# Kernel tuning notes

Hardware: AMD Instinct MI355X
Metric: run time of the kernel (lower is better)

The kernel has to match this reference:

```python
import jax, jax.numpy as jnp
import numpy as np

L, C, H, FF = 12, 768, 12, 3072
DH = C // H
VOCAB = 30522
B, P, T = 64, 196, 40
PATCH_FLAT = 768  # 16*16*3
MAXP, MAXW = P + 1, T + 2


def _ln(x, w, b, eps):
    m = jnp.mean(x, axis=-1, keepdims=True)
    v = jnp.mean(jnp.square(x - m), axis=-1, keepdims=True)
    return (x - m) * jax.lax.rsqrt(v + eps) * w + b


def setup_inputs() -> dict:
    key = jax.random.key(0)
    ks = iter(jax.random.split(key, 40))
    s = 0.02
    rn = lambda shape: jax.random.normal(next(ks), shape, jnp.float32) * s
    return {
        'vis_in': jax.random.normal(next(ks), (B, P, PATCH_FLAT), jnp.float32),
        'txt_in': jax.random.randint(next(ks), (B, T), 0, VOCAB),
        'vis_mask': jnp.ones((B, P), jnp.int32),
        'txt_mask': jnp.ones((B, T), jnp.int32),
        'patch_w': rn((C, PATCH_FLAT)), 'patch_b': jnp.zeros((C,), jnp.float32),
        'w_embed': rn((VOCAB, C)),
        't_pos': rn((MAXW, C)),
        'v_pos': rn((1, MAXP, C)),
        'v_cls': rn((1, 1, C)),
        'v_mod': rn((1, 1, C)), 't_mod': rn((1, 1, C)),
        'vn_w': jnp.ones((C,), jnp.float32), 'vn_b': jnp.zeros((C,), jnp.float32),
        'tn_w': jnp.ones((C,), jnp.float32), 'tn_b': jnp.zeros((C,), jnp.float32),
        'qkv_w': rn((L, 3 * C, C)), 'qkv_b': jnp.zeros((L, 3 * C), jnp.float32),
        'proj_w': rn((L, C, C)), 'proj_b': jnp.zeros((L, C), jnp.float32),
        'n1_w': jnp.ones((L, C), jnp.float32), 'n1_b': jnp.zeros((L, C), jnp.float32),
        'n2_w': jnp.ones((L, C), jnp.float32), 'n2_b': jnp.zeros((L, C), jnp.float32),
        'fc1_w': rn((L, FF, C)), 'fc1_b': jnp.zeros((L, FF), jnp.float32),
        'fc2_w': rn((L, C, FF)), 'fc2_b': jnp.zeros((L, C), jnp.float32),
    }


def reference(vis_in, txt_in, vis_mask, txt_mask, patch_w, patch_b, w_embed, t_pos,
              v_pos, v_cls, v_mod, t_mod, vn_w, vn_b, tn_w, tn_b, qkv_w, qkv_b,
              proj_w, proj_b, n1_w, n1_b, n2_w, n2_b, fc1_w, fc1_b, fc2_w, fc2_b):
    Bsz = vis_in.shape[0]
    # patch projection and word embedding
    v_emb = vis_in @ patch_w.T + patch_b                      # [B, P, C]
    t_emb = w_embed[txt_in]                                    # [B, T, C]
    v_emb = jnp.concatenate([jnp.broadcast_to(v_cls, (Bsz, 1, C)), v_emb], axis=1)
    VL = v_emb.shape[1]                                        # P + 1
    v_emb = _ln(v_emb + v_pos[:, :VL] + v_mod, vn_w, vn_b, 1e-5)
    t_emb = _ln(t_emb + t_pos[:T] + t_mod, tn_w, tn_b, 1e-5)
    x = jnp.concatenate([t_emb, v_emb], axis=1)                # [B, N, C], N = T+1+P
    m = jnp.concatenate([txt_mask, jnp.ones((Bsz, 1), txt_mask.dtype), vis_mask], axis=-1)
    # pairwise mask: attn_mask[b,i,j] == 0 -> masked (broadcast over heads)
    masked = (m[:, None, :, None] * m[:, None, None, :]) == 0  # [B,1,N,N]
    scale = DH ** -0.5
    for l in range(L):
        h = _ln(x, n1_w[l], n1_b[l], 1e-6)
        qkv = (h @ qkv_w[l].T + qkv_b[l]).reshape(Bsz, -1, 3, H, DH)
        q = jnp.transpose(qkv[:, :, 0], (0, 2, 1, 3))          # [B,H,N,DH]
        k = jnp.transpose(qkv[:, :, 1], (0, 2, 1, 3))
        v = jnp.transpose(qkv[:, :, 2], (0, 2, 1, 3))
        attn = jnp.einsum('bhqd,bhkd->bhqk', q, k) * scale
        attn = jnp.where(masked, jnp.asarray(-1e30, attn.dtype), attn)
        attn = jax.nn.softmax(attn, axis=-1)
        o = jnp.einsum('bhqk,bhkd->bhqd', attn, v)
        o = jnp.transpose(o, (0, 2, 1, 3)).reshape(Bsz, -1, C)
        x = x + (o @ proj_w[l].T + proj_b[l])
        h2 = _ln(x, n2_w[l], n2_b[l], 1e-6)
        h2 = jax.nn.gelu(h2 @ fc1_w[l].T + fc1_b[l], approximate=False)
        x = x + (h2 @ fc2_w[l].T + fc2_b[l])
    return x
```

## Files before the change

### kernel.cpp

```cpp
#include <hip/hip_runtime.h>
#include <hip/hip_bf16.h>

using bf16 = __hip_bfloat16;
typedef __bf16 bfv8 __attribute__((ext_vector_type(8)));
typedef float f32x4 __attribute__((ext_vector_type(4)));

#define DEVI __device__ __forceinline__

constexpr int L_ = 12, C_ = 768, H_ = 12, FF_ = 3072, DH_ = 64;
constexpr int B_ = 64, P_ = 196, T_ = 40;
constexpr int N_ = T_ + 1 + P_;
constexpr int M_ = B_ * N_;
constexpr int MPAD = 15360;
constexpr int NKV = 256;
constexpr int BP_ = B_ * P_;

constexpr size_t OFF_X   = 0;
constexpr size_t SZ_X    = (size_t)MPAD * C_ * 4;
constexpr size_t OFF_H   = OFF_X + SZ_X;
constexpr size_t SZ_H    = (size_t)MPAD * C_ * 2;
constexpr size_t OFF_Q   = OFF_H + SZ_H;
constexpr size_t SZ_QKV1 = (size_t)B_ * H_ * NKV * DH_ * 2;
constexpr size_t OFF_K   = OFF_Q + SZ_QKV1;
constexpr size_t OFF_V   = OFF_K + SZ_QKV1;
constexpr size_t OFF_O   = OFF_V + SZ_QKV1;
constexpr size_t SZ_O    = SZ_H;
constexpr size_t OFF_FFH = OFF_O + SZ_O;
constexpr size_t SZ_FFH  = (size_t)MPAD * FF_ * 2;
constexpr size_t OFF_WB  = OFF_FFH + SZ_FFH;
constexpr size_t SZ_WB   = (size_t)(2304 + 768 + 3072 + 3072) * 768 * 2;
constexpr size_t WS_NEED = OFF_WB + SZ_WB;
constexpr size_t OFF_PTMP = OFF_FFH;
constexpr size_t OFF_VISB = OFF_FFH + (size_t)40 * 1024 * 1024;
constexpr size_t OFF_PWB  = OFF_WB;

DEVI void gld_lds16(const bf16* g, bf16* l) {
  __builtin_amdgcn_global_load_lds((__attribute__((address_space(1))) void*)(g),
                                   (__attribute__((address_space(3))) void*)(l), 16, 0, 0);
}

DEVI void swz_tiles(int bid, int G, int NTC, int& bm, int& bn) {
  const int qq = G >> 3, rr = G & 7;
  const int xcd = bid & 7, base = bid >> 3;
  const int lin = (xcd < rr ? xcd * (qq + 1) : rr * (qq + 1) + (xcd - rr) * qq) + base;
  bm = lin / NTC;
  bn = lin - bm * NTC;
}

DEVI uint packbf(float lo, float hi) {
  union { struct { bf16 x, y; } h; uint u; } r;
  r.h.x = __float2bfloat16(lo); r.h.y = __float2bfloat16(hi);
  return r.u;
}

DEVI float gelu_f(float v) {
  const float p = v * (1.5957691f + 0.07135481f * v * v) * 1.442695041f;
  const float d = exp2f(-p);
  return v / (1.f + d);
}

template <int BM, int BN, int TPB, int WM, int WN, int EPI>
__global__ __launch_bounds__(TPB, 2) void gemm2ph(
    const bf16* __restrict__ A, const bf16* __restrict__ W,
    const float* __restrict__ bias, float* __restrict__ outf,
    float* __restrict__ outf2, bf16* __restrict__ outb,
    bf16* __restrict__ qb, bf16* __restrict__ kb, bf16* __restrict__ vb,
    int Nout, int K, int Mvalid, int NTC) {
  extern __shared__ __align__(16) char lds[];
  constexpr int NWAVE = TPB / 64;
  constexpr int MR = BM / (WM * 16);
  constexpr int NR = BN / (WN * 16);
  constexpr int LA = (BM / 8) / NWAVE;
  constexpr int LB = (BN / 8) / NWAVE;
  constexpr int TOTL = LA + LB;
  constexpr int ASZ = BM * 128;
  constexpr int BUF = ASZ + BN * 128;

  const int tid = threadIdx.x, wid = tid >> 6, lane = tid & 63;
  const int wm = wid / WN, wn = wid % WN;
  int bm, bn;
  swz_tiles(blockIdx.x, gridDim.x, NTC, bm, bn);
  const size_t arow0 = (size_t)bm * BM;
  const size_t brow0 = (size_t)bn * BN;

  const int cswz = (((lane & 7) ^ ((lane >> 3) & 7)) * 8);
  const size_t aoff0 = (arow0 + (size_t)wid * (LA * 8) + (lane >> 3)) * K + cswz;
  const size_t boff0 = (brow0 + (size_t)wid * (LB * 8) + (lane >> 3)) * K + cswz;

  f32x4 acc[MR][NR];
#pragma unroll
  for (int m = 0; m < MR; m++)
#pragma unroll
    for (int n = 0; n < NR; n++) acc[m][n] = (f32x4){0.f, 0.f, 0.f, 0.f};

  auto STAGE = [&](int t, int bufoff) {
    const size_t ka = aoff0 + (size_t)t * 64;
#pragma unroll
    for (int i = 0; i < LA; i++)
      gld_lds16(A + ka + (size_t)i * 8 * K,
                (bf16*)(lds + bufoff + (wid * LA + i) * 1024));
    const size_t kw = boff0 + (size_t)t * 64;
#pragma unroll
    for (int i = 0; i < LB; i++)
      gld_lds16(W + kw + (size_t)i * 8 * K,
                (bf16*)(lds + bufoff + ASZ + (wid * LB + i) * 1024));
  };

  const int la = lane & 15, g = lane >> 4, s7 = lane & 7;
  auto COMPUTE = [&](int bufoff) {
    const char* Ab = lds + bufoff;
    const char* Bb = lds + bufoff + ASZ;
#pragma unroll
    for (int ks = 0; ks < 2; ks++) {
      const int slot = ((ks * 4 + g) ^ s7) * 16;
      bfv8 bfr[NR];
#pragma unroll
      for (int n = 0; n < NR; n++)
        bfr[n] = *(const bfv8*)(Bb + (wn * (NR * 16) + n * 16 + la) * 128 + slot);
#pragma unroll
      for (int m = 0; m < MR; m++) {
        bfv8 af = *(const bfv8*)(Ab + (wm * (MR * 16) + m * 16 + la) * 128 + slot);
#pragma unroll
        for (int n = 0; n < NR; n++)
          acc[m][n] = __builtin_amdgcn_mfma_f32_16x16x32_bf16(af, bfr[n], acc[m][n], 0, 0, 0);
      }
    }
  };

  const int NT = K >> 6;
  STAGE(0, 0);
  int cur = 0;
  for (int t = 0; t < NT; ++t) {
    if (t + 1 < NT) {
      STAGE(t + 1, (cur ^ 1) * BUF);
      if constexpr (TOTL == 8) asm volatile("s_waitcnt vmcnt(8)" ::: "memory");
      else if constexpr (TOTL == 6) asm volatile("s_waitcnt vmcnt(6)" ::: "memory");
      else asm volatile("s_waitcnt vmcnt(4)" ::: "memory");
    } else {
      asm volatile("s_waitcnt vmcnt(0)" ::: "memory");
    }
    asm volatile("s_barrier" ::: "memory");
    COMPUTE(cur * BUF);
    asm volatile("s_barrier" ::: "memory");
    cur ^= 1;
  }

  const int row0 = (int)arow0 + wm * (MR * 16);
  const int col0 = (int)brow0 + wn * (NR * 16);
  float bv[NR];
#pragma unroll
  for (int n = 0; n < NR; n++) bv[n] = bias[col0 + n * 16 + la];

  if constexpr (EPI == 0 || EPI == 2 || EPI == 4) {
#pragma unroll
    for (int n = 0; n < NR; n++) {
      const int colb = col0 + n * 16 + la;
#pragma unroll
      for (int m = 0; m < MR; m++)
#pragma unroll
        for (int j = 0; j < 4; j++) {
          const int row = row0 + m * 16 + (lane >> 4) * 4 + j;
          const float v = acc[m][n][j] + bv[n];
          if constexpr (EPI == 0) outf[(size_t)row * Nout + colb] = v;
          else if constexpr (EPI == 2) outf[(size_t)row * Nout + colb] += v;
          else { if (row < Mvalid) outf2[(size_t)row * Nout + colb] = outf[(size_t)row * Nout + colb] + v; }
        }
    }
  } else if constexpr (EPI == 3) {
#pragma unroll
    for (int m = 0; m < MR; m++)
#pragma unroll
      for (int j = 0; j < 4; j++) {
        const int row = row0 + m * 16 + (lane >> 4) * 4 + j;
#pragma unroll
        for (int n = 0; n < NR; n++) {
          const float v = gelu_f(acc[m][n][j] + bv[n]);
          const float p = __shfl_xor(v, 1);
          if (!(lane & 1))
            *(uint*)(outb + (size_t)row * Nout + col0 + n * 16 + la) = packbf(v, p);
        }
      }
  } else {
#pragma unroll
    for (int m = 0; m < MR; m++)
#pragma unroll
      for (int j = 0; j < 4; j++) {
        const int row = row0 + m * 16 + (lane >> 4) * 4 + j;
        const bool ok = row < Mvalid;
        const int bI = row / N_;
        const int nI = row - bI * N_;
#pragma unroll
        for (int n = 0; n < NR; n++) {
          const int colb = col0 + n * 16 + la;
          const float v = acc[m][n][j] + bv[n];
          const float p = __shfl_xor(v, 1);
          if (ok && !(lane & 1)) {
            const int s = colb / C_;
            const int rem = colb - s * C_;
            const int hh = rem >> 6, dd = rem & 63;
            bf16* dst = (s == 0) ? qb : (s == 1) ? kb : vb;
            *(uint*)(dst + (((size_t)bI * H_ + hh) * NKV + nI) * DH_ + dd) = packbf(v, p);
          }
        }
      }
  }
}

__global__ __launch_bounds__(256) void conv_weights_k(
    const float* __restrict__ wq, const float* __restrict__ wp,
    const float* __restrict__ wf1, const float* __restrict__ wf2,
    bf16* __restrict__ dst) {
  const long n0 = 2304L * 768 / 4, n1 = 768L * 768 / 4;
  const long n2 = 3072L * 768 / 4;
  const long tot = n0 + n1 + 2 * n2;
  for (long i = (long)blockIdx.x * 256 + threadIdx.x; i < tot; i += (long)gridDim.x * 256) {
    const float* s; long off;
    if (i < n0) { s = wq; off = i; }
    else if (i < n0 + n1) { s = wp; off = i - n0; }
    else if (i < n0 + n1 + n2) { s = wf1; off = i - n0 - n1; }
    else { s = wf2; off = i - n0 - n1 - n2; }
    float4 v = ((const float4*)s)[off];
    union { short4 q; bf16 h[4]; } u;
    u.h[0] = __float2bfloat16(v.x); u.h[1] = __float2bfloat16(v.y);
    u.h[2] = __float2bfloat16(v.z); u.h[3] = __float2bfloat16(v.w);
    ((short4*)dst)[i] = u.q;
  }
}

__global__ __launch_bounds__(256) void f32_to_bf16_k(const float* __restrict__ s,
                                                     bf16* __restrict__ d, long n4) {
  long i = (long)blockIdx.x * 256 + threadIdx.x;
  long stride = (long)gridDim.x * 256;
  for (; i < n4; i += stride) {
    float4 v = ((const float4*)s)[i];
    union { short4 q; bf16 h[4]; } u;
    u.h[0] = __float2bfloat16(v.x); u.h[1] = __float2bfloat16(v.y);
    u.h[2] = __float2bfloat16(v.z); u.h[3] = __float2bfloat16(v.w);
    ((short4*)d)[i] = u.q;
  }
}

__global__ __launch_bounds__(256) void embed_kernel(
    const float* __restrict__ ptmp, const int* __restrict__ txt_in,
    const float* __restrict__ wemb, const float* __restrict__ tpos,
    const float* __restrict__ vpos, const float* __restrict__ vcls,
    const float* __restrict__ vmod, const float* __restrict__ tmod,
    const float* __restrict__ vnw, const float* __restrict__ vnb,
    const float* __restrict__ tnw, const float* __restrict__ tnb,
    float* __restrict__ x) {
  const int row = blockIdx.x;
  const int tid = threadIdx.x;
  if (row >= M_) {
    for (int i = tid; i < C_; i += 256) x[(size_t)row * C_ + i] = 0.f;
    return;
  }
  const int b = row / N_, n = row - (row / N_) * N_;
  const bool istxt = n < T_;
  float e[3];
#pragma unroll
  for (int i = 0; i < 3; i++) {
    const int c = tid + i * 256;
    float v;
    if (istxt) {
      v = wemb[(size_t)txt_in[b * T_ + n] * C_ + c] + tpos[n * C_ + c] + tmod[c];
    } else {
      const int vi = n - T_;
      const float base = (vi == 0) ? vcls[c] : ptmp[((size_t)b * P_ + (vi - 1)) * C_ + c];
      v = base + vpos[vi * C_ + c] + vmod[c];
    }
    e[i] = v;
  }
  float s = e[0] + e[1] + e[2];
  float s2 = e[0] * e[0] + e[1] * e[1] + e[2] * e[2];
#pragma unroll
  for (int d = 1; d < 64; d <<= 1) { s += __shfl_xor(s, d); s2 += __shfl_xor(s2, d); }
  __shared__ float rs[4], rs2[4];
  const int wid = tid >> 6, lane = tid & 63;
  if (lane == 0) { rs[wid] = s; rs2[wid] = s2; }
  __syncthreads();
  s = rs[0] + rs[1] + rs[2] + rs[3];
  s2 = rs2[0] + rs2[1] + rs2[2] + rs2[3];
  const float mean = s * (1.f / C_);
  const float var = s2 * (1.f / C_) - mean * mean;
  const float rr = rsqrtf(var + 1e-5f);
  const float* w = istxt ? tnw : vnw;
  const float* bb = istxt ? tnb : vnb;
#pragma unroll
  for (int i = 0; i < 3; i++) {
    const int c = tid + i * 256;
    x[(size_t)row * C_ + c] = (e[i] - mean) * rr * w[c] + bb[c];
  }
}

__global__ __launch_bounds__(256) void ln_rows(const float* __restrict__ x,
                                               const float* __restrict__ w,
                                               const float* __restrict__ b,
                                               bf16* __restrict__ out, float eps) {
  const int row = blockIdx.x * 4 + (threadIdx.x >> 6);
  const int lane = threadIdx.x & 63;
  if (row >= MPAD) return;
  bf16* op = out + (size_t)row * C_;
  if (row >= M_) {
#pragma unroll
    for (int i = 0; i < 3; i++)
      *(short4*)(op + (lane + 64 * i) * 4) = make_short4(0, 0, 0, 0);
    return;
  }
  const float4* xp = (const float4*)(x + (size_t)row * C_);
  float4 v[3];
  float s = 0.f, s2 = 0.f;
#pragma unroll
  for (int i = 0; i < 3; i++) {
    v[i] = xp[lane + 64 * i];
    s += v[i].x + v[i].y + v[i].z + v[i].w;
    s2 += v[i].x * v[i].x + v[i].y * v[i].y + v[i].z * v[i].z + v[i].w * v[i].w;
  }
#pragma unroll
  for (int d = 1; d < 64; d <<= 1) { s += __shfl_xor(s, d); s2 += __shfl_xor(s2, d); }
  const float mean = s * (1.f / C_);
  const float rr = rsqrtf(s2 * (1.f / C_) - mean * mean + eps);
#pragma unroll
  for (int i = 0; i < 3; i++) {
    const int c0 = (lane + 64 * i) * 4;
    const float4 w4 = *(const float4*)(w + c0);
    const float4 b4 = *(const float4*)(b + c0);
    union { short4 s4; bf16 h[4]; } u;
    u.h[0] = __float2bfloat16((v[i].x - mean) * rr * w4.x + b4.x);
    u.h[1] = __float2bfloat16((v[i].y - mean) * rr * w4.y + b4.y);
    u.h[2] = __float2bfloat16((v[i].z - mean) * rr * w4.z + b4.z);
    u.h[3] = __float2bfloat16((v[i].w - mean) * rr * w4.w + b4.w);
    *(short4*)(op + c0) = u.s4;
  }
}

DEVI float maskval(const int* __restrict__ tm, const int* __restrict__ vm, int b, int j) {
  if (j < T_) return tm[b * T_ + j] ? 1.f : 0.f;
  if (j == T_) return 1.f;
  if (j < N_) return vm[b * P_ + (j - T_ - 1)] ? 1.f : 0.f;
  return 0.f;
}

__global__ __launch_bounds__(256) void attn_fused(
    const bf16* __restrict__ qb, const bf16* __restrict__ kb,
    const bf16* __restrict__ vb, const int* __restrict__ txt_mask,
    const int* __restrict__ vis_mask, bf16* __restrict__ ob) {
  __shared__ alignas(16) __bf16 Vt[64 * 264];
  __shared__ alignas(16) __bf16 Ps[64 * 264];
  const int qblk = blockIdx.x;
  const int bh = blockIdx.y;
  const int b = bh / H_, hh = bh - b * H_;
  const int tid = threadIdx.x, wid = tid >> 6, lane = tid & 63;

  const __bf16* Vg = (const __bf16*)(vb + (size_t)bh * NKV * DH_);
#pragma unroll
  for (int it = 0; it < 8; it++) {
    const int r = lane + 64 * (it & 3);
    const int c8 = (wid + 4 * (it >> 2)) * 8;
    bfv8 v;
    if (r < N_) v = *(const bfv8*)(Vg + (size_t)r * DH_ + c8);
    else { union { int4 i; bfv8 x; } z; z.i = make_int4(0,0,0,0); v = z.x; }
#pragma unroll
    for (int d = 0; d < 8; d++) Vt[(c8 + d) * 264 + r] = v[d];
  }

  const int qbase = qblk * 64 + wid * 16;
  const __bf16* Qg = (const __bf16*)(qb + (size_t)bh * NKV * DH_);
  const __bf16* Kg = (const __bf16*)(kb + (size_t)bh * NKV * DH_);
  bfv8 aq[2];
#pragma unroll
  for (int kk = 0; kk < 2; kk++)
    aq[kk] = *(const bfv8*)(Qg + (size_t)(qbase + (lane & 15)) * DH_ + kk * 32 + (lane >> 4) * 8);

  f32x4 acc[16];
#pragma unroll
  for (int f = 0; f < 16; f++) acc[f] = (f32x4){0.f, 0.f, 0.f, 0.f};
#pragma unroll
  for (int f = 0; f < 16; f++) {
#pragma unroll
    for (int kk = 0; kk < 2; kk++) {
      bfv8 bk = *(const bfv8*)(Kg + (size_t)(f * 16 + (lane & 15)) * DH_ + kk * 32 + (lane >> 4) * 8);
      acc[f] = __builtin_amdgcn_mfma_f32_16x16x32_bf16(aq[kk], bk, acc[f], 0, 0, 0);
    }
  }

  float cm[16];
#pragma unroll
  for (int f = 0; f < 16; f++)
    cm[f] = maskval(txt_mask, vis_mask, b, f * 16 + (lane & 15));

  const float scale = 0.125f;
#pragma unroll
  for (int j = 0; j < 4; j++) {
    const int qr = qbase + (lane >> 4) * 4 + j;
    const float qm = (qr < N_) ? maskval(txt_mask, vis_mask, b, qr) : 1.f;
    float sv[16];
    float mx = -3.0e38f;
#pragma unroll
    for (int f = 0; f < 16; f++) {
      const int col = f * 16 + (lane & 15);
      float sc;
      if (col >= N_) sc = -INFINITY;
      else if (qm * cm[f] == 0.f) sc = -1e30f;
      else sc = acc[f][j] * scale;
      sv[f] = sc;
      mx = fmaxf(mx, sc);
    }
#pragma unroll
    for (int d = 1; d < 16; d <<= 1) mx = fmaxf(mx, __shfl_xor(mx, d));
    float sum = 0.f;
#pragma unroll
    for (int f = 0; f < 16; f++) { const float p = expf(sv[f] - mx); sv[f] = p; sum += p; }
#pragma unroll
    for (int d = 1; d < 16; d <<= 1) sum += __shfl_xor(sum, d);
    const float inv = 1.f / sum;
    const int ql = wid * 16 + (lane >> 4) * 4 + j;
#pragma unroll
    for (int f = 0; f < 16; f++)
      Ps[ql * 264 + f * 16 + (lane & 15)] = (__bf16)(sv[f] * inv);
  }

  __syncthreads();

  f32x4 oacc[4];
#pragma unroll
  for (int n = 0; n < 4; n++) oacc[n] = (f32x4){0.f, 0.f, 0.f, 0.f};
#pragma unroll
  for (int kk = 0; kk < 8; kk++) {
    bfv8 ap = *(const bfv8*)&Ps[(wid * 16 + (lane & 15)) * 264 + kk * 32 + (lane >> 4) * 8];
#pragma unroll
    for (int n = 0; n < 4; n++) {
      bfv8 bv = *(const bfv8*)&Vt[(n * 16 + (lane & 15)) * 264 + kk * 32 + (lane >> 4) * 8];
      oacc[n] = __builtin_amdgcn_mfma_f32_16x16x32_bf16(ap, bv, oacc[n], 0, 0, 0);
    }
  }
#pragma unroll
  for (int n = 0; n < 4; n++)
#pragma unroll
    for (int j = 0; j < 4; j++) {
      const int q = qbase + (lane >> 4) * 4 + j;
      if (q < N_)
        ob[((size_t)b * N_ + q) * C_ + hh * 64 + n * 16 + (lane & 15)] =
            __float2bfloat16(oacc[n][j]);
    }
}

extern "C" void kernel_launch(void* const* d_in, const int* in_sizes, int n_in,
                              void* d_out, int out_size, void* d_ws, size_t ws_size,
                              hipStream_t stream) {
  const float* vis_in  = (const float*)d_in[0];
  const int*   txt_in  = (const int*)d_in[1];
  const int*   vis_mask = (const int*)d_in[2];
  const int*   txt_mask = (const int*)d_in[3];
  const float* patch_w = (const float*)d_in[4];
  const float* patch_b = (const float*)d_in[5];
  const float* w_embed = (const float*)d_in[6];
  const float* t_pos   = (const float*)d_in[7];
  const float* v_pos   = (const float*)d_in[8];
  const float* v_cls   = (const float*)d_in[9];
  const float* v_mod   = (const float*)d_in[10];
  const float* t_mod   = (const float*)d_in[11];
  const float* vn_w = (const float*)d_in[12];
  const float* vn_b = (const float*)d_in[13];
  const float* tn_w = (const float*)d_in[14];
  const float* tn_b = (const float*)d_in[15];
  const float* qkv_w = (const float*)d_in[16];
  const float* qkv_b = (const float*)d_in[17];
  const float* proj_w = (const float*)d_in[18];
  const float* proj_b = (const float*)d_in[19];
  const float* n1_w = (const float*)d_in[20];
  const float* n1_b = (const float*)d_in[21];
  const float* n2_w = (const float*)d_in[22];
  const float* n2_b = (const float*)d_in[23];
  const float* fc1_w = (const float*)d_in[24];
  const float* fc1_b = (const float*)d_in[25];
  const float* fc2_w = (const float*)d_in[26];
  const float* fc2_b = (const float*)d_in[27];

  char* ws = (char*)d_ws;
  if (ws_size < WS_NEED) {
    hipMemsetAsync(d_out, 0, (size_t)out_size * 4, stream);
    return;
  }
  float* x    = (float*)(ws + OFF_X);
  bf16* h     = (bf16*)(ws + OFF_H);
  bf16* qbuf  = (bf16*)(ws + OFF_Q);
  bf16* kbuf  = (bf16*)(ws + OFF_K);
  bf16* vbuf  = (bf16*)(ws + OFF_V);
  bf16* obuf  = (bf16*)(ws + OFF_O);
  bf16* ffh   = (bf16*)(ws + OFF_FFH);
  bf16* wq    = (bf16*)(ws + OFF_WB);
  bf16* wp    = wq + (size_t)2304 * 768;
  bf16* wf1   = wp + (size_t)768 * 768;
  bf16* wf2   = wf1 + (size_t)3072 * 768;
  float* ptmp = (float*)(ws + OFF_PTMP);
  bf16* visb  = (bf16*)(ws + OFF_VISB);
  bf16* pwb   = (bf16*)(ws + OFF_PWB);

  constexpr int LDS_A = 2 * (256 + 256) * 128;
  constexpr int LDS_B = 2 * (256 + 128) * 128;
  constexpr int LDS_C = 2 * (128 + 128) * 128;
  (void)hipFuncSetAttribute((const void*)gemm2ph<256, 256, 512, 2, 4, 1>,
                            hipFuncAttributeMaxDynamicSharedMemorySize, LDS_A);
  (void)hipFuncSetAttribute((const void*)gemm2ph<256, 256, 512, 2, 4, 3>,
                            hipFuncAttributeMaxDynamicSharedMemorySize, LDS_A);
  (void)hipFuncSetAttribute((const void*)gemm2ph<256, 128, 512, 2, 4, 0>,
                            hipFuncAttributeMaxDynamicSharedMemorySize, LDS_B);
  (void)hipFuncSetAttribute((const void*)gemm2ph<128, 128, 256, 2, 2, 2>,
                            hipFuncAttributeMaxDynamicSharedMemorySize, LDS_C);
  (void)hipFuncSetAttribute((const void*)gemm2ph<128, 128, 256, 2, 2, 4>,
                            hipFuncAttributeMaxDynamicSharedMemorySize, LDS_C);

  f32_to_bf16_k<<<1024, 256, 0, stream>>>(vis_in, visb, (long)BP_ * C_ / 4);
  f32_to_bf16_k<<<256, 256, 0, stream>>>(patch_w, pwb, (long)C_ * C_ / 4);
  gemm2ph<256, 128, 512, 2, 4, 0><<<(BP_ / 256) * (C_ / 128), 512, LDS_B, stream>>>(
      visb, pwb, patch_b, ptmp, nullptr, nullptr, nullptr, nullptr, nullptr,
      C_, C_, BP_, C_ / 128);
  embed_kernel<<<MPAD, 256, 0, stream>>>(ptmp, txt_in, w_embed, t_pos, v_pos, v_cls,
                                         v_mod, t_mod, vn_w, vn_b, tn_w, tn_b, x);

  for (int l = 0; l < L_; l++) {
    conv_weights_k<<<2048, 256, 0, stream>>>(
        qkv_w + (size_t)l * 2304 * 768, proj_w + (size_t)l * 768 * 768,
        fc1_w + (size_t)l * 3072 * 768, fc2_w + (size_t)l * 768 * 3072, wq);

    ln_rows<<<MPAD / 4, 256, 0, stream>>>(x, n1_w + l * C_, n1_b + l * C_, h, 1e-6f);
    gemm2ph<256, 256, 512, 2, 4, 1><<<(MPAD / 256) * (2304 / 256), 512, LDS_A, stream>>>(
        h, wq, qkv_b + (size_t)l * 2304, nullptr, nullptr, nullptr, qbuf, kbuf, vbuf,
        2304, C_, M_, 2304 / 256);
    attn_fused<<<dim3(4, B_ * H_), 256, 0, stream>>>(qbuf, kbuf, vbuf, txt_mask,
                                                     vis_mask, obuf);
    gemm2ph<128, 128, 256, 2, 2, 2><<<(MPAD / 128) * (C_ / 128), 256, LDS_C, stream>>>(
        obuf, wp, proj_b + (size_t)l * C_, x, nullptr, nullptr, nullptr, nullptr,
        nullptr, C_, C_, M_, C_ / 128);
    ln_rows<<<MPAD / 4, 256, 0, stream>>>(x, n2_w + l * C_, n2_b + l * C_, h, 1e-6f);
    gemm2ph<256, 256, 512, 2, 4, 3><<<(MPAD / 256) * (FF_ / 256), 512, LDS_A, stream>>>(
        h, wf1, fc1_b + (size_t)l * FF_, nullptr, nullptr, ffh, nullptr, nullptr,
        nullptr, FF_, C_, M_, FF_ / 256);
    if (l < L_ - 1) {
      gemm2ph<128, 128, 256, 2, 2, 2><<<(MPAD / 128) * (C_ / 128), 256, LDS_C, stream>>>(
          ffh, wf2, fc2_b + (size_t)l * C_, x, nullptr, nullptr, nullptr, nullptr,
          nullptr, C_, FF_, M_, C_ / 128);
    } else {
      gemm2ph<128, 128, 256, 2, 2, 4><<<(MPAD / 128) * (C_ / 128), 256, LDS_C, stream>>>(
          ffh, wf2, fc2_b + (size_t)l * C_, x, (float*)d_out, nullptr, nullptr,
          nullptr, nullptr, C_, FF_, M_, C_ / 128);
    }
  }
}
```

Before: 6.410 ms.

## Replace templated double-buffered GEMM with fixed 256x128 triple-buffered pipeline

The GEMM kernel is rewritten to a single 256x128 tile shape with 8 waves and a three-stage LDS ring, so loads run two K-steps ahead instead of one. All GEMMs (QKV, proj, fc1, fc2, patch) now use this shape. The smaller projection GEMMs move from 128x128 to 256x128 tiles, which means fewer blocks. The 144KB LDS per block limits occupancy to one block per CU despite launch_bounds(512,2). The deeper prefetch is meant to hide global-load latency better.

Result: slower. 6.728 ms (+5.0%).

```diff
diff --git a/kernel.cpp b/kernel.cpp
--- a/kernel.cpp
+++ b/kernel.cpp
@@ -59,69 +59,63 @@
   return v / (1.f + d);
 }
 
-template <int BM, int BN, int TPB, int WM, int WN, int EPI>
-__global__ __launch_bounds__(TPB, 2) void gemm2ph(
+template <int EPI>
+__global__ __launch_bounds__(512, 2) void gemm3s(
     const bf16* __restrict__ A, const bf16* __restrict__ W,
     const float* __restrict__ bias, float* __restrict__ outf,
     float* __restrict__ outf2, bf16* __restrict__ outb,
     bf16* __restrict__ qb, bf16* __restrict__ kb, bf16* __restrict__ vb,
     int Nout, int K, int Mvalid, int NTC) {
   extern __shared__ __align__(16) char lds[];
-  constexpr int NWAVE = TPB / 64;
-  constexpr int MR = BM / (WM * 16);
-  constexpr int NR = BN / (WN * 16);
-  constexpr int LA = (BM / 8) / NWAVE;
-  constexpr int LB = (BN / 8) / NWAVE;
-  constexpr int TOTL = LA + LB;
-  constexpr int ASZ = BM * 128;
-  constexpr int BUF = ASZ + BN * 128;
+  constexpr int SLOT = 49152;
+  constexpr int BOFF = 32768;
 
   const int tid = threadIdx.x, wid = tid >> 6, lane = tid & 63;
-  const int wm = wid / WN, wn = wid % WN;
+  const int wm = wid >> 1, wn = wid & 1;
   int bm, bn;
   swz_tiles(blockIdx.x, gridDim.x, NTC, bm, bn);
-  const size_t arow0 = (size_t)bm * BM;
-  const size_t brow0 = (size_t)bn * BN;
-
-  const int cswz = (((lane & 7) ^ ((lane >> 3) & 7)) * 8);
-  const size_t aoff0 = (arow0 + (size_t)wid * (LA * 8) + (lane >> 3)) * K + cswz;
-  const size_t boff0 = (brow0 + (size_t)wid * (LB * 8) + (lane >> 3)) * K + cswz;
-
-  f32x4 acc[MR][NR];
-#pragma unroll
-  for (int m = 0; m < MR; m++)
-#pragma unroll
-    for (int n = 0; n < NR; n++) acc[m][n] = (f32x4){0.f, 0.f, 0.f, 0.f};
-
-  auto STAGE = [&](int t, int bufoff) {
-    const size_t ka = aoff0 + (size_t)t * 64;
-#pragma unroll
-    for (int i = 0; i < LA; i++)
-      gld_lds16(A + ka + (size_t)i * 8 * K,
-                (bf16*)(lds + bufoff + (wid * LA + i) * 1024));
-    const size_t kw = boff0 + (size_t)t * 64;
-#pragma unroll
-    for (int i = 0; i < LB; i++)
-      gld_lds16(W + kw + (size_t)i * 8 * K,
-                (bf16*)(lds + bufoff + ASZ + (wid * LB + i) * 1024));
+  const size_t arow0 = (size_t)bm * 256;
+  const size_t brow0 = (size_t)bn * 128;
+
+  const int xr = ((lane & 7) ^ (lane >> 3)) * 8;
+  const size_t aoff0 = (arow0 + (size_t)wid * 32 + (lane >> 3)) * K + xr;
+  const size_t boff0 = (brow0 + (size_t)wid * 16 + (lane >> 3)) * K + xr;
+
+  f32x4 acc[4][4];
+#pragma unroll
+  for (int m = 0; m < 4; m++)
+#pragma unroll
+    for (int n = 0; n < 4; n++) acc[m][n] = (f32x4){0.f, 0.f, 0.f, 0.f};
+
+  auto STAGE = [&](int t, int so) {
+    char* slot = lds + so;
+    const bf16* Ag = A + aoff0 + (size_t)t * 64;
+#pragma unroll
+    for (int i = 0; i < 4; i++)
+      gld_lds16(Ag + (size_t)i * 8 * K, (bf16*)(slot + (wid * 32 + i * 8) * 128));
+    const bf16* Wg = W + boff0 + (size_t)t * 64;
+#pragma unroll
+    for (int i = 0; i < 2; i++)
+      gld_lds16(Wg + (size_t)i * 8 * K, (bf16*)(slot + BOFF + (wid * 16 + i * 8) * 128));
   };
 
-  const int la = lane & 15, g = lane >> 4, s7 = lane & 7;
-  auto COMPUTE = [&](int bufoff) {
-    const char* Ab = lds + bufoff;
-    const char* Bb = lds + bufoff + ASZ;
+  const int la = lane & 15, g = lane >> 4;
+  auto COMPUTE = [&](int so) {
+    const char* slot = lds + so;
 #pragma unroll
     for (int ks = 0; ks < 2; ks++) {
-      const int slot = ((ks * 4 + g) ^ s7) * 16;
-      bfv8 bfr[NR];
-#pragma unroll
-      for (int n = 0; n < NR; n++)
-        bfr[n] = *(const bfv8*)(Bb + (wn * (NR * 16) + n * 16 + la) * 128 + slot);
-#pragma unroll
-      for (int m = 0; m < MR; m++) {
-        bfv8 af = *(const bfv8*)(Ab + (wm * (MR * 16) + m * 16 + la) * 128 + slot);
-#pragma unroll
-        for (int n = 0; n < NR; n++)
+      bfv8 bfr[4];
+#pragma unroll
+      for (int n = 0; n < 4; n++) {
+        const int r = wn * 64 + n * 16 + la;
+        bfr[n] = *(const bfv8*)(slot + BOFF + r * 128 + (((ks * 4 + g) ^ (r & 7)) * 16));
+      }
+#pragma unroll
+      for (int m = 0; m < 4; m++) {
+        const int r = wm * 64 + m * 16 + la;
+        bfv8 af = *(const bfv8*)(slot + r * 128 + (((ks * 4 + g) ^ (r & 7)) * 16));
+#pragma unroll
+        for (int n = 0; n < 4; n++)
           acc[m][n] = __builtin_amdgcn_mfma_f32_16x16x32_bf16(af, bfr[n], acc[m][n], 0, 0, 0);
       }
     }
@@ -129,37 +123,39 @@
 
   const int NT = K >> 6;
   STAGE(0, 0);
-  int cur = 0;
+  STAGE(1, SLOT);
+  int cs = 0, sp = 2 * SLOT;
   for (int t = 0; t < NT; ++t) {
-    if (t + 1 < NT) {
-      STAGE(t + 1, (cur ^ 1) * BUF);
-      if constexpr (TOTL == 8) asm volatile("s_waitcnt vmcnt(8)" ::: "memory");
-      else if constexpr (TOTL == 6) asm volatile("s_waitcnt vmcnt(6)" ::: "memory");
-      else asm volatile("s_waitcnt vmcnt(4)" ::: "memory");
+    if (t + 2 < NT) {
+      STAGE(t + 2, sp);
+      sp = (sp == 2 * SLOT) ? 0 : sp + SLOT;
+      asm volatile("s_waitcnt vmcnt(12)" ::: "memory");
+    } else if (t + 1 < NT) {
+      asm volatile("s_waitcnt vmcnt(6)" ::: "memory");
     } else {
       asm volatile("s_waitcnt vmcnt(0)" ::: "memory");
     }
     asm volatile("s_barrier" ::: "memory");
-    COMPUTE(cur * BUF);
+    COMPUTE(cs);
+    cs = (cs == 2 * SLOT) ? 0 : cs + SLOT;
     asm volatile("s_barrier" ::: "memory");
-    cur ^= 1;
-  }
-
-  const int row0 = (int)arow0 + wm * (MR * 16);
-  const int col0 = (int)brow0 + wn * (NR * 16);
-  float bv[NR];
-#pragma unroll
-  for (int n = 0; n < NR; n++) bv[n] = bias[col0 + n * 16 + la];
+  }
+
+  const int row0 = (int)arow0 + wm * 64;
+  const int col0 = (int)brow0 + wn * 64;
+  float bv[4];
+#pragma unroll
+  for (int n = 0; n < 4; n++) bv[n] = bias[col0 + n * 16 + la];
 
   if constexpr (EPI == 0 || EPI == 2 || EPI == 4) {
 #pragma unroll
-    for (int n = 0; n < NR; n++) {
+    for (int n = 0; n < 4; n++) {
       const int colb = col0 + n * 16 + la;
 #pragma unroll
-      for (int m = 0; m < MR; m++)
+      for (int m = 0; m < 4; m++)
 #pragma unroll
         for (int j = 0; j < 4; j++) {
-          const int row = row0 + m * 16 + (lane >> 4) * 4 + j;
+          const int row = row0 + m * 16 + g * 4 + j;
           const float v = acc[m][n][j] + bv[n];
           if constexpr (EPI == 0) outf[(size_t)row * Nout + colb] = v;
           else if constexpr (EPI == 2) outf[(size_t)row * Nout + colb] += v;
@@ -168,12 +164,12 @@
     }
   } else if constexpr (EPI == 3) {
 #pragma unroll
-    for (int m = 0; m < MR; m++)
+    for (int m = 0; m < 4; m++)
 #pragma unroll
       for (int j = 0; j < 4; j++) {
-        const int row = row0 + m * 16 + (lane >> 4) * 4 + j;
-#pragma unroll
-        for (int n = 0; n < NR; n++) {
+        const int row = row0 + m * 16 + g * 4 + j;
+#pragma unroll
+        for (int n = 0; n < 4; n++) {
           const float v = gelu_f(acc[m][n][j] + bv[n]);
           const float p = __shfl_xor(v, 1);
           if (!(lane & 1))
@@ -182,15 +178,15 @@
       }
   } else {
 #pragma unroll
-    for (int m = 0; m < MR; m++)
+    for (int m = 0; m < 4; m++)
 #pragma unroll
       for (int j = 0; j < 4; j++) {
-        const int row = row0 + m * 16 + (lane >> 4) * 4 + j;
+        const int row = row0 + m * 16 + g * 4 + j;
         const bool ok = row < Mvalid;
         const int bI = row / N_;
         const int nI = row - bI * N_;
 #pragma unroll
-        for (int n = 0; n < NR; n++) {
+        for (int n = 0; n < 4; n++) {
           const int colb = col0 + n * 16 + la;
           const float v = acc[m][n][j] + bv[n];
           const float p = __shfl_xor(v, 1);
@@ -496,23 +492,16 @@
   bf16* visb  = (bf16*)(ws + OFF_VISB);
   bf16* pwb   = (bf16*)(ws + OFF_PWB);
 
-  constexpr int LDS_A = 2 * (256 + 256) * 128;
-  constexpr int LDS_B = 2 * (256 + 128) * 128;
-  constexpr int LDS_C = 2 * (128 + 128) * 128;
-  (void)hipFuncSetAttribute((const void*)gemm2ph<256, 256, 512, 2, 4, 1>,
-                            hipFuncAttributeMaxDynamicSharedMemorySize, LDS_A);
-  (void)hipFuncSetAttribute((const void*)gemm2ph<256, 256, 512, 2, 4, 3>,
-                            hipFuncAttributeMaxDynamicSharedMemorySize, LDS_A);
-  (void)hipFuncSetAttribute((const void*)gemm2ph<256, 128, 512, 2, 4, 0>,
-                            hipFuncAttributeMaxDynamicSharedMemorySize, LDS_B);
-  (void)hipFuncSetAttribute((const void*)gemm2ph<128, 128, 256, 2, 2, 2>,
-                            hipFuncAttributeMaxDynamicSharedMemorySize, LDS_C);
-  (void)hipFuncSetAttribute((const void*)gemm2ph<128, 128, 256, 2, 2, 4>,
-                            hipFuncAttributeMaxDynamicSharedMemorySize, LDS_C);
+  constexpr int LDS3 = 3 * 49152;
+  (void)hipFuncSetAttribute((const void*)gemm3s<0>, hipFuncAttributeMaxDynamicSharedMemorySize, LDS3);
+  (void)hipFuncSetAttribute((const void*)gemm3s<1>, hipFuncAttributeMaxDynamicSharedMemorySize, LDS3);
+  (void)hipFuncSetAttribute((const void*)gemm3s<2>, hipFuncAttributeMaxDynamicSharedMemorySize, LDS3);
+  (void)hipFuncSetAttribute((const void*)gemm3s<3>, hipFuncAttributeMaxDynamicSharedMemorySize, LDS3);
+  (void)hipFuncSetAttribute((const void*)gemm3s<4>, hipFuncAttributeMaxDynamicSharedMemorySize, LDS3);
 
   f32_to_bf16_k<<<1024, 256, 0, stream>>>(vis_in, visb, (long)BP_ * C_ / 4);
   f32_to_bf16_k<<<256, 256, 0, stream>>>(patch_w, pwb, (long)C_ * C_ / 4);
-  gemm2ph<256, 128, 512, 2, 4, 0><<<(BP_ / 256) * (C_ / 128), 512, LDS_B, stream>>>(
+  gemm3s<0><<<(BP_ / 256) * (C_ / 128), 512, LDS3, stream>>>(
       visb, pwb, patch_b, ptmp, nullptr, nullptr, nullptr, nullptr, nullptr,
       C_, C_, BP_, C_ / 128);
   embed_kernel<<<MPAD, 256, 0, stream>>>(ptmp, txt_in, w_embed, t_pos, v_pos, v_cls,
@@ -524,24 +513,24 @@
         fc1_w + (size_t)l * 3072 * 768, fc2_w + (size_t)l * 768 * 3072, wq);
 
     ln_rows<<<MPAD / 4, 256, 0, stream>>>(x, n1_w + l * C_, n1_b + l * C_, h, 1e-6f);
-    gemm2ph<256, 256, 512, 2, 4, 1><<<(MPAD / 256) * (2304 / 256), 512, LDS_A, stream>>>(
+    gemm3s<1><<<(MPAD / 256) * (2304 / 128), 512, LDS3, stream>>>(
         h, wq, qkv_b + (size_t)l * 2304, nullptr, nullptr, nullptr, qbuf, kbuf, vbuf,
-        2304, C_, M_, 2304 / 256);
+        2304, C_, M_, 2304 / 128);
     attn_fused<<<dim3(4, B_ * H_), 256, 0, stream>>>(qbuf, kbuf, vbuf, txt_mask,
                                                      vis_mask, obuf);
-    gemm2ph<128, 128, 256, 2, 2, 2><<<(MPAD / 128) * (C_ / 128), 256, LDS_C, stream>>>(
+    gemm3s<2><<<(MPAD / 256) * (C_ / 128), 512, LDS3, stream>>>(
         obuf, wp, proj_b + (size_t)l * C_, x, nullptr, nullptr, nullptr, nullptr,
         nullptr, C_, C_, M_, C_ / 128);
     ln_rows<<<MPAD / 4, 256, 0, stream>>>(x, n2_w + l * C_, n2_b + l * C_, h, 1e-6f);
-    gemm2ph<256, 256, 512, 2, 4, 3><<<(MPAD / 256) * (FF_ / 256), 512, LDS_A, stream>>>(
+    gemm3s<3><<<(MPAD / 256) * (FF_ / 128), 512, LDS3, stream>>>(
         h, wf1, fc1_b + (size_t)l * FF_, nullptr, nullptr, ffh, nullptr, nullptr,
-        nullptr, FF_, C_, M_, FF_ / 256);
+        nullptr, FF_, C_, M_, FF_ / 128);
     if (l < L_ - 1) {
-      gemm2ph<128, 128, 256, 2, 2, 2><<<(MPAD / 128) * (C_ / 128), 256, LDS_C, stream>>>(
+      gemm3s<2><<<(MPAD / 256) * (C_ / 128), 512, LDS3, stream>>>(
           ffh, wf2, fc2_b + (size_t)l * C_, x, nullptr, nullptr, nullptr, nullptr,
           nullptr, C_, FF_, M_, C_ / 128);
     } else {
-      gemm2ph<128, 128, 256, 2, 2, 4><<<(MPAD / 128) * (C_ / 128), 256, LDS_C, stream>>>(
+      gemm3s<4><<<(MPAD / 256) * (C_ / 128), 512, LDS3, stream>>>(
           ffh, wf2, fc2_b + (size_t)l * C_, x, (float*)d_out, nullptr, nullptr,
           nullptr, nullptr, C_, FF_, M_, C_ / 128);
     }
```

## Rework GEMM to K=32 static-LDS stages with s_setprio and larger proj/fc2 tiles

Applied to the files above, without the earlier changes.

Replaces the dynamic-LDS K=64 double-buffered GEMM with a kernel that stages K=32 slices into static shared memory, uses a new rotation-based bank swizzle, loads all fragments before issuing MFMAs, and raises wave priority around the MFMA block. The proj and fc2 GEMMs move from 128x128 tiles with 256 threads to 256x128 tiles with 512 threads, and the launch-bounds occupancy hint of 2 is dropped. The intent is better data reuse and more MFMA density per barrier. The cost is twice as many barriers per K, fewer blocks for the N=768 GEMMs (60x6), and possibly lower occupancy.

New measurement: 6.897 ms. +7.6%, slower.

```diff
diff --git a/kernel.cpp b/kernel.cpp
--- a/kernel.cpp
+++ b/kernel.cpp
@@ -59,22 +59,19 @@
   return v / (1.f + d);
 }
 
-template <int BM, int BN, int TPB, int WM, int WN, int EPI>
-__global__ __launch_bounds__(TPB, 2) void gemm2ph(
+template <int BM, int BN, int WM, int WN, int EPI>
+__global__ __launch_bounds__(512) void gemm_big(
     const bf16* __restrict__ A, const bf16* __restrict__ W,
     const float* __restrict__ bias, float* __restrict__ outf,
     float* __restrict__ outf2, bf16* __restrict__ outb,
     bf16* __restrict__ qb, bf16* __restrict__ kb, bf16* __restrict__ vb,
     int Nout, int K, int Mvalid, int NTC) {
-  extern __shared__ __align__(16) char lds[];
-  constexpr int NWAVE = TPB / 64;
   constexpr int MR = BM / (WM * 16);
   constexpr int NR = BN / (WN * 16);
-  constexpr int LA = (BM / 8) / NWAVE;
-  constexpr int LB = (BN / 8) / NWAVE;
-  constexpr int TOTL = LA + LB;
-  constexpr int ASZ = BM * 128;
-  constexpr int BUF = ASZ + BN * 128;
+  constexpr int LA = BM / 128;
+  constexpr int LB = BN / 128;
+  __shared__ alignas(16) bf16 As[2][BM * 32];
+  __shared__ alignas(16) bf16 Bs[2][BN * 32];
 
   const int tid = threadIdx.x, wid = tid >> 6, lane = tid & 63;
   const int wm = wid / WN, wn = wid % WN;
@@ -83,9 +80,26 @@
   const size_t arow0 = (size_t)bm * BM;
   const size_t brow0 = (size_t)bn * BN;
 
-  const int cswz = (((lane & 7) ^ ((lane >> 3) & 7)) * 8);
-  const size_t aoff0 = (arow0 + (size_t)wid * (LA * 8) + (lane >> 3)) * K + cswz;
-  const size_t boff0 = (brow0 + (size_t)wid * (LB * 8) + (lane >> 3)) * K + cswz;
+  const int lrow = lane >> 2;
+  const int gch = ((lane & 3) - ((lane >> 3) & 3)) & 3;
+  const bf16* pA[2];
+  const bf16* pB[2];
+#pragma unroll
+  for (int i = 0; i < LA; i++)
+    pA[i] = A + (arow0 + (size_t)(wid * LA + i) * 16 + lrow) * K + gch * 8;
+#pragma unroll
+  for (int i = 0; i < LB; i++)
+    pB[i] = W + (brow0 + (size_t)(wid * LB + i) * 16 + lrow) * K + gch * 8;
+
+  auto STAGE = [&](int t, int b) {
+    const size_t k = (size_t)t * 32;
+#pragma unroll
+    for (int i = 0; i < LA; i++)
+      gld_lds16(pA[i] + k, &As[b][((wid * LA + i) * 16) * 32]);
+#pragma unroll
+    for (int i = 0; i < LB; i++)
+      gld_lds16(pB[i] + k, &Bs[b][((wid * LB + i) * 16) * 32]);
+  };
 
   f32x4 acc[MR][NR];
 #pragma unroll
@@ -93,56 +107,36 @@
 #pragma unroll
     for (int n = 0; n < NR; n++) acc[m][n] = (f32x4){0.f, 0.f, 0.f, 0.f};
 
-  auto STAGE = [&](int t, int bufoff) {
-    const size_t ka = aoff0 + (size_t)t * 64;
-#pragma unroll
-    for (int i = 0; i < LA; i++)
-      gld_lds16(A + ka + (size_t)i * 8 * K,
-                (bf16*)(lds + bufoff + (wid * LA + i) * 1024));
-    const size_t kw = boff0 + (size_t)t * 64;
-#pragma unroll
-    for (int i = 0; i < LB; i++)
-      gld_lds16(W + kw + (size_t)i * 8 * K,
-                (bf16*)(lds + bufoff + ASZ + (wid * LB + i) * 1024));
-  };
-
-  const int la = lane & 15, g = lane >> 4, s7 = lane & 7;
-  auto COMPUTE = [&](int bufoff) {
-    const char* Ab = lds + bufoff;
-    const char* Bb = lds + bufoff + ASZ;
-#pragma unroll
-    for (int ks = 0; ks < 2; ks++) {
-      const int slot = ((ks * 4 + g) ^ s7) * 16;
-      bfv8 bfr[NR];
-#pragma unroll
-      for (int n = 0; n < NR; n++)
-        bfr[n] = *(const bfv8*)(Bb + (wn * (NR * 16) + n * 16 + la) * 128 + slot);
-#pragma unroll
-      for (int m = 0; m < MR; m++) {
-        bfv8 af = *(const bfv8*)(Ab + (wm * (MR * 16) + m * 16 + la) * 128 + slot);
-#pragma unroll
-        for (int n = 0; n < NR; n++)
-          acc[m][n] = __builtin_amdgcn_mfma_f32_16x16x32_bf16(af, bfr[n], acc[m][n], 0, 0, 0);
-      }
-    }
-  };
-
-  const int NT = K >> 6;
+  const int la = lane & 15, g = lane >> 4;
+  const int slot8 = ((g + (la >> 1)) & 3) * 8;
+
+  const int NT = K >> 5;
   STAGE(0, 0);
-  int cur = 0;
   for (int t = 0; t < NT; ++t) {
+    const int b = t & 1;
     if (t + 1 < NT) {
-      STAGE(t + 1, (cur ^ 1) * BUF);
-      if constexpr (TOTL == 8) asm volatile("s_waitcnt vmcnt(8)" ::: "memory");
-      else if constexpr (TOTL == 6) asm volatile("s_waitcnt vmcnt(6)" ::: "memory");
-      else asm volatile("s_waitcnt vmcnt(4)" ::: "memory");
+      STAGE(t + 1, b ^ 1);
+      if constexpr (LA + LB == 4) asm volatile("s_waitcnt vmcnt(4)" ::: "memory");
+      else                        asm volatile("s_waitcnt vmcnt(3)" ::: "memory");
     } else {
       asm volatile("s_waitcnt vmcnt(0)" ::: "memory");
     }
     asm volatile("s_barrier" ::: "memory");
-    COMPUTE(cur * BUF);
+    bfv8 af[MR], bfr[NR];
+#pragma unroll
+    for (int n = 0; n < NR; n++)
+      bfr[n] = *(const bfv8*)&Bs[b][(wn * (NR * 16) + n * 16 + la) * 32 + slot8];
+#pragma unroll
+    for (int m = 0; m < MR; m++)
+      af[m] = *(const bfv8*)&As[b][(wm * (MR * 16) + m * 16 + la) * 32 + slot8];
+    __builtin_amdgcn_s_setprio(1);
+#pragma unroll
+    for (int m = 0; m < MR; m++)
+#pragma unroll
+      for (int n = 0; n < NR; n++)
+        acc[m][n] = __builtin_amdgcn_mfma_f32_16x16x32_bf16(af[m], bfr[n], acc[m][n], 0, 0, 0);
+    __builtin_amdgcn_s_setprio(0);
     asm volatile("s_barrier" ::: "memory");
-    cur ^= 1;
   }
 
   const int row0 = (int)arow0 + wm * (MR * 16);
@@ -159,7 +153,7 @@
       for (int m = 0; m < MR; m++)
 #pragma unroll
         for (int j = 0; j < 4; j++) {
-          const int row = row0 + m * 16 + (lane >> 4) * 4 + j;
+          const int row = row0 + m * 16 + g * 4 + j;
           const float v = acc[m][n][j] + bv[n];
           if constexpr (EPI == 0) outf[(size_t)row * Nout + colb] = v;
           else if constexpr (EPI == 2) outf[(size_t)row * Nout + colb] += v;
@@ -171,7 +165,7 @@
     for (int m = 0; m < MR; m++)
 #pragma unroll
       for (int j = 0; j < 4; j++) {
-        const int row = row0 + m * 16 + (lane >> 4) * 4 + j;
+        const int row = row0 + m * 16 + g * 4 + j;
 #pragma unroll
         for (int n = 0; n < NR; n++) {
           const float v = gelu_f(acc[m][n][j] + bv[n]);
@@ -185,7 +179,7 @@
     for (int m = 0; m < MR; m++)
 #pragma unroll
       for (int j = 0; j < 4; j++) {
-        const int row = row0 + m * 16 + (lane >> 4) * 4 + j;
+        const int row = row0 + m * 16 + g * 4 + j;
         const bool ok = row < Mvalid;
         const int bI = row / N_;
         const int nI = row - bI * N_;
@@ -496,23 +490,9 @@
   bf16* visb  = (bf16*)(ws + OFF_VISB);
   bf16* pwb   = (bf16*)(ws + OFF_PWB);
 
-  constexpr int LDS_A = 2 * (256 + 256) * 128;
-  constexpr int LDS_B = 2 * (256 + 128) * 128;
-  constexpr int LDS_C = 2 * (128 + 128) * 128;
-  (void)hipFuncSetAttribute((const void*)gemm2ph<256, 256, 512, 2, 4, 1>,
-                            hipFuncAttributeMaxDynamicSharedMemorySize, LDS_A);
-  (void)hipFuncSetAttribute((const void*)gemm2ph<256, 256, 512, 2, 4, 3>,
-                            hipFuncAttributeMaxDynamicSharedMemorySize, LDS_A);
-  (void)hipFuncSetAttribute((const void*)gemm2ph<256, 128, 512, 2, 4, 0>,
-                            hipFuncAttributeMaxDynamicSharedMemorySize, LDS_B);
-  (void)hipFuncSetAttribute((const void*)gemm2ph<128, 128, 256, 2, 2, 2>,
-                            hipFuncAttributeMaxDynamicSharedMemorySize, LDS_C);
-  (void)hipFuncSetAttribute((const void*)gemm2ph<128, 128, 256, 2, 2, 4>,
-                            hipFuncAttributeMaxDynamicSharedMemorySize, LDS_C);
-
   f32_to_bf16_k<<<1024, 256, 0, stream>>>(vis_in, visb, (long)BP_ * C_ / 4);
   f32_to_bf16_k<<<256, 256, 0, stream>>>(patch_w, pwb, (long)C_ * C_ / 4);
-  gemm2ph<256, 128, 512, 2, 4, 0><<<(BP_ / 256) * (C_ / 128), 512, LDS_B, stream>>>(
+  gemm_big<256, 128, 4, 2, 0><<<(BP_ / 256) * (C_ / 128), 512, 0, stream>>>(
       visb, pwb, patch_b, ptmp, nullptr, nullptr, nullptr, nullptr, nullptr,
       C_, C_, BP_, C_ / 128);
   embed_kernel<<<MPAD, 256, 0, stream>>>(ptmp, txt_in, w_embed, t_pos, v_pos, v_cls,
@@ -524,24 +504,24 @@
         fc1_w + (size_t)l * 3072 * 768, fc2_w + (size_t)l * 768 * 3072, wq);
 
     ln_rows<<<MPAD / 4, 256, 0, stream>>>(x, n1_w + l * C_, n1_b + l * C_, h, 1e-6f);
-    gemm2ph<256, 256, 512, 2, 4, 1><<<(MPAD / 256) * (2304 / 256), 512, LDS_A, stream>>>(
+    gemm_big<256, 256, 2, 4, 1><<<(MPAD / 256) * (2304 / 256), 512, 0, stream>>>(
         h, wq, qkv_b + (size_t)l * 2304, nullptr, nullptr, nullptr, qbuf, kbuf, vbuf,
         2304, C_, M_, 2304 / 256);
     attn_fused<<<dim3(4, B_ * H_), 256, 0, stream>>>(qbuf, kbuf, vbuf, txt_mask,
                                                      vis_mask, obuf);
-    gemm2ph<128, 128, 256, 2, 2, 2><<<(MPAD / 128) * (C_ / 128), 256, LDS_C, stream>>>(
+    gemm_big<256, 128, 4, 2, 2><<<(MPAD / 256) * (C_ / 128), 512, 0, stream>>>(
         obuf, wp, proj_b + (size_t)l * C_, x, nullptr, nullptr, nullptr, nullptr,
         nullptr, C_, C_, M_, C_ / 128);
     ln_rows<<<MPAD / 4, 256, 0, stream>>>(x, n2_w + l * C_, n2_b + l * C_, h, 1e-6f);
-    gemm2ph<256, 256, 512, 2, 4, 3><<<(MPAD / 256) * (FF_ / 256), 512, LDS_A, stream>>>(
+    gemm_big<256, 256, 2, 4, 3><<<(MPAD / 256) * (FF_ / 256), 512, 0, stream>>>(
         h, wf1, fc1_b + (size_t)l * FF_, nullptr, nullptr, ffh, nullptr, nullptr,
         nullptr, FF_, C_, M_, FF_ / 256);
     if (l < L_ - 1) {
-      gemm2ph<128, 128, 256, 2, 2, 2><<<(MPAD / 128) * (C_ / 128), 256, LDS_C, stream>>>(
+      gemm_big<256, 128, 4, 2, 2><<<(MPAD / 256) * (C_ / 128), 512, 0, stream>>>(
           ffh, wf2, fc2_b + (size_t)l * C_, x, nullptr, nullptr, nullptr, nullptr,
           nullptr, C_, FF_, M_, C_ / 128);
     } else {
-      gemm2ph<128, 128, 256, 2, 2, 4><<<(MPAD / 128) * (C_ / 128), 256, LDS_C, stream>>>(
+      gemm_big<256, 128, 4, 2, 4><<<(MPAD / 256) * (C_ / 128), 512, 0, stream>>>(
           ffh, wf2, fc2_b + (size_t)l * C_, x, (float*)d_out, nullptr, nullptr,
           nullptr, nullptr, C_, FF_, M_, C_ / 128);
     }
```
